# Kernel optimization log

Hardware: AMD Instinct MI355X
Metric: run time of the kernel (lower is better)

The kernel has to match this reference:

```python
import jax, jax.numpy as jnp
import numpy as np

H, DM, DX = 4, 64, 64  # num_heads, out_m_dim, out_x_dim
IN_L, IN_M, IN_X = 128, 128, 128
N, E, E2 = 10000, 160000, 320000


def _edge_softmax(scores, dst, num_nodes):
    # scores: [n_edges, H, 1]; softmax over edges sharing the same dst node
    mx = jax.ops.segment_max(scores, dst, num_segments=num_nodes)
    ex = jnp.exp(scores - mx[dst])
    denom = jax.ops.segment_sum(ex, dst, num_segments=num_nodes)
    return ex / denom[dst]


def setup_inputs() -> dict:
    key = jax.random.key(0)
    ks = jax.random.split(key, 24)

    def xn(k, shape):
        fan = sum(shape)
        return jax.random.normal(k, shape, dtype=jnp.float32) * np.sqrt(2.0 / fan)

    inp = {
        'l_feats': jax.random.normal(ks[0], (N, IN_L), dtype=jnp.float32),
        'm_feats': jax.random.normal(ks[1], (E, IN_M), dtype=jnp.float32),
        'x_feats': jax.random.normal(ks[2], (E2, IN_X), dtype=jnp.float32),
        'g_src': jax.random.randint(ks[3], (E,), 0, N, dtype=jnp.int32),
        'g_dst': jax.random.randint(ks[4], (E,), 0, N, dtype=jnp.int32),
        'lg_src': jax.random.randint(ks[5], (E2,), 0, E, dtype=jnp.int32),
        'lg_dst': jax.random.randint(ks[6], (E2,), 0, E, dtype=jnp.int32),
        # line-graph branch params (torch Linear convention: W [out, in])
        'W_lg_node': xn(ks[7], (DM * H, IN_M + IN_X)),
        'b_lg_node': jnp.zeros((DM * H,), dtype=jnp.float32),
        'W_lg_ni': xn(ks[8], (DX * H, IN_M)),
        'W_lg_fij': xn(ks[9], (DX * H, IN_X)),
        'W_lg_nj': xn(ks[10], (DX * H, IN_M)),
        'lg_attn': xn(ks[11], (1, H, DX)),
        'bias_lg': jnp.zeros((H * DX,), dtype=jnp.float32),
        # base-graph branch params
        'W_g_node': xn(ks[12], (DM * H, IN_M + IN_L)),
        'b_g_node': jnp.zeros((DM * H,), dtype=jnp.float32),
        'W_g_ni': xn(ks[13], (DM * H, IN_L)),
        'W_g_fij': xn(ks[14], (DM * H, IN_M)),
        'W_g_nj': xn(ks[15], (DM * H, IN_L)),
        'g_attn': xn(ks[16], (1, H, DM)),
        'bias_g': jnp.zeros((H * DM,), dtype=jnp.float32),
    }
    return inp


def reference(l_feats, m_feats, x_feats,
              W_lg_node, b_lg_node, W_lg_ni, W_lg_fij, W_lg_nj, lg_attn, bias_lg,
              W_g_node, b_g_node, W_g_ni, W_g_fij, W_g_nj, g_attn, bias_g,
              g_src, g_dst, lg_src, lg_dst):
    n_nodes = l_feats.shape[0]      # graph nodes
    n_lnodes = m_feats.shape[0]     # l_graph nodes == graph edges
    lrelu = jax.nn.leaky_relu       # slope 0.01 (torch default)

    # ---- line-graph attention branch ----
    lg_f_ni = m_feats @ W_lg_ni.T                      # [E, H*DX]
    lg_f_nj = m_feats @ W_lg_nj.T
    lg_f_fij = x_feats @ W_lg_fij.T                    # [E2, H*DX]
    lg_f_out = lrelu(lg_f_ni[lg_src] + lg_f_nj[lg_dst] + lg_f_fij + bias_lg)
    xr = lg_f_out.reshape(-1, H, DX)                   # [E2, H, DX]
    lg_e = jnp.sum(xr * lg_attn, axis=-1, keepdims=True)  # [E2, H, 1]
    a_lg = _edge_softmax(lg_e, lg_dst, n_lnodes)       # [E2, H, 1]

    # mean-aggregate l_graph edge feats onto dst nodes (DGL send_and_recv mean)
    cnt = jax.ops.segment_sum(jnp.ones((lg_dst.shape[0],), dtype=x_feats.dtype),
                              lg_dst, num_segments=n_lnodes)
    agg = jax.ops.segment_sum(x_feats, lg_dst, num_segments=n_lnodes)
    agg = agg / jnp.maximum(cnt, 1.0)[:, None]         # [E, IN_X]

    m1 = jnp.concatenate([m_feats, agg], axis=1)       # [E, IN_M+IN_X]
    h1 = (m1 @ W_lg_node.T + b_lg_node).reshape(-1, H, DM)
    msg1 = h1[lg_src] * a_lg                           # u_mul_e
    h1_dst = jax.ops.segment_sum(msg1, lg_dst, num_segments=n_lnodes)
    lg_h_out = jnp.sum(lrelu(h1_dst), axis=1)          # [E, DM]

    # ---- base-graph attention branch ----
    g_f_ni = l_feats @ W_g_ni.T                        # [N, H*DM]
    g_f_nj = l_feats @ W_g_nj.T
    g_f_fij = m_feats @ W_g_fij.T                      # [E, H*DM]
    g_f_out = lrelu(g_f_ni[g_src] + g_f_nj[g_dst] + g_f_fij + bias_g)
    g_f_out = g_f_out.reshape(-1, H, DM)               # [E, H, DM]
    g_e = jnp.sum(g_f_out * g_attn, axis=-1, keepdims=True)  # [E, H, 1]

    node_edge = l_feats[g_src] + l_feats[g_dst]        # [E, IN_L]
    m2 = jnp.concatenate([node_edge, m_feats], axis=1)  # [E, IN_L+IN_M]
    h2 = (m2 @ W_g_node.T + b_g_node).reshape(-1, H, DM)
    a_g = _edge_softmax(g_e, g_dst, n_nodes)           # [E, H, 1] (per graph edge)
    # l_graph.update_all(u_mul_v): msg[e2] = h2[src(e2)] * a_g[dst(e2)]
    msg2 = h2[lg_src] * a_g[lg_dst]
    h2_dst = jax.ops.segment_sum(msg2, lg_dst, num_segments=n_lnodes)
    g_h_out = jnp.sum(lrelu(h2_dst), axis=1)           # [E, DM]

    return g_h_out + lg_h_out                          # [E, DM]
```

## Files before the change

kernel.cpp:

```cpp
#include <hip/hip_runtime.h>
#include <math.h>

#define LRELU(x) ((x) > 0.0f ? (x) : 0.01f * (x))

typedef __attribute__((ext_vector_type(8))) short short8;
typedef __attribute__((ext_vector_type(4))) float f32x4;

__device__ __forceinline__ unsigned fenc(float f) {
    unsigned u = __float_as_uint(f);
    return (u & 0x80000000u) ? ~u : (u | 0x80000000u);
}
__device__ __forceinline__ float fdec(unsigned u) {
    return __uint_as_float((u & 0x80000000u) ? (u & 0x7FFFFFFFu) : ~u);
}
__device__ __forceinline__ unsigned short f2bf(float f) {
    unsigned u = __float_as_uint(f);
    u += 0x7FFFu + ((u >> 16) & 1u);
    return (unsigned short)(u >> 16);
}
__device__ __forceinline__ float bf2f(unsigned short b) {
    return __uint_as_float(((unsigned)b) << 16);
}
__device__ __forceinline__ ushort4 cvt4(float4 v) {
    ushort4 p;
    p.x = f2bf(v.x); p.y = f2bf(v.y); p.z = f2bf(v.z); p.w = f2bf(v.w);
    return p;
}

__global__ __launch_bounds__(256) void wcvt_k(
    const float* __restrict__ s0, const float* __restrict__ s1,
    const float* __restrict__ s2, const float* __restrict__ s3,
    const float* __restrict__ s4, const float* __restrict__ s5,
    const float* __restrict__ s6, const float* __restrict__ s7,
    unsigned short* __restrict__ dst)
{
    long long e = ((long long)blockIdx.x * 256 + threadIdx.x) * 4;
    if (e >= 327680) return;
    int c = (int)(e >> 15);
    const float* s;
    long long off = e & 32767;
    switch (c) {
        case 0: s = s0; break;
        case 1: s = s1; break;
        case 2: s = s2; break;
        case 3: s = s3; break;
        case 4: s = s4; break;
        case 5: s = s5; break;
        case 6: s = s6; break;
        case 7: s = s6; off += 32768; break;
        case 8: s = s7; break;
        default: s = s7; off += 32768; break;
    }
    float4 v = *(const float4*)&s[off];
    *(ushort4*)&dst[e] = cvt4(v);
}

__global__ __launch_bounds__(256) void cvt1_k(
    const float* __restrict__ in, unsigned short* __restrict__ out, int n4)
{
    int stride = gridDim.x * 256;
    for (int u = blockIdx.x * 256 + threadIdx.x; u < n4; u += stride) {
        float4 v = *(const float4*)&in[(size_t)u * 4];
        *(ushort4*)&out[(size_t)u * 4] = cvt4(v);
    }
}

__device__ __forceinline__ void stage_A128(
    unsigned short* __restrict__ smem, const void* __restrict__ Av, int is_bf16,
    int row0, int M, int tid, int col_off, int stride)
{
    if (is_bf16) {
        const unsigned short* A = (const unsigned short*)Av;
        short8 v[4];
#pragma unroll
        for (int k = 0; k < 4; ++k) {
            int j = tid + k * 256;
            int r = row0 + (j >> 4);
#pragma unroll
            for (int q = 0; q < 8; ++q) v[k][q] = 0;
            if (r < M) v[k] = *(const short8*)&A[(size_t)r * 128 + (j & 15) * 8];
        }
#pragma unroll
        for (int k = 0; k < 4; ++k) {
            int j = tid + k * 256;
            *(short8*)&smem[(j >> 4) * stride + col_off + (j & 15) * 8] = v[k];
        }
    } else {
        const float* A = (const float*)Av;
        float4 va[8];
#pragma unroll
        for (int k = 0; k < 8; ++k) {
            int i = tid + k * 256;
            int r = row0 + (i >> 5);
            va[k] = make_float4(0.f, 0.f, 0.f, 0.f);
            if (r < M) va[k] = *(const float4*)&A[(size_t)r * 128 + (i & 31) * 4];
        }
#pragma unroll
        for (int k = 0; k < 8; ++k) {
            int i = tid + k * 256;
            *(ushort4*)&smem[(i >> 5) * stride + col_off + (i & 31) * 4] = cvt4(va[k]);
        }
    }
}

__global__ __launch_bounds__(256) void gemm128_mfma(
    const void* __restrict__ Av, int a_is_bf16,
    const unsigned short* __restrict__ Wbf,
    const float* __restrict__ biasf, unsigned short* __restrict__ Cout, int M)
{
    __shared__ __align__(16) unsigned short smem[64 * 264];
    const int row0 = blockIdx.x * 64;
    const int tid = threadIdx.x;
    const int wv = tid >> 6, lane = tid & 63;
    const int ln = lane & 15, quad = lane >> 4;

    stage_A128(smem, Av, a_is_bf16, row0, M, tid, 0, 136);
    __syncthreads();

    f32x4 acc[16];
#pragma unroll
    for (int t = 0; t < 16; ++t) acc[t] = (f32x4){0.f, 0.f, 0.f, 0.f};

#pragma unroll 1
    for (int ks = 0; ks < 4; ++ks) {
        short8 a = *(const short8*)&smem[(wv * 16 + ln) * 136 + ks * 32 + quad * 8];
#pragma unroll
        for (int t = 0; t < 16; ++t) {
            short8 b = *(const short8*)&Wbf[(size_t)(t * 16 + ln) * 128 + ks * 32 + quad * 8];
            acc[t] = __builtin_amdgcn_mfma_f32_16x16x32_bf16(a, b, acc[t], 0, 0, 0);
        }
    }
    __syncthreads();

#pragma unroll
    for (int t = 0; t < 16; ++t) {
        int col = t * 16 + ln;
        float bb = biasf ? biasf[col] : 0.0f;
#pragma unroll
        for (int rg = 0; rg < 4; ++rg)
            smem[(wv * 16 + quad * 4 + rg) * 264 + col] = f2bf(acc[t][rg] + bb);
    }
    __syncthreads();
#pragma unroll 1
    for (int i = tid; i < 2048; i += 256) {
        int row = i >> 5, c8 = (i & 31) * 8;
        int r = row0 + row;
        if (r < M) *(short8*)&Cout[(size_t)r * 256 + c8] = *(const short8*)&smem[row * 264 + c8];
    }
}

__global__ __launch_bounds__(256) void gemm_score_mfma(
    const void* __restrict__ Av, int a_is_bf16,
    const unsigned short* __restrict__ Wbf,
    const unsigned short* __restrict__ fni, const unsigned short* __restrict__ fnj,
    const float* __restrict__ bias, const float* __restrict__ attn,
    const int* __restrict__ src, const int* __restrict__ dst,
    float* __restrict__ ebuf, unsigned* __restrict__ smax, int M)
{
    __shared__ __align__(16) unsigned short smem[64 * 264];
    const int row0 = blockIdx.x * 64;
    const int tid = threadIdx.x;
    const int wv = tid >> 6, lane = tid & 63;
    const int ln = lane & 15, quad = lane >> 4;

    const int myr = row0 + wv * 16 + ln;
    int msrc = 0, mdst = 0;
    if (myr < M) { msrc = src[myr]; mdst = dst[myr]; }

    stage_A128(smem, Av, a_is_bf16, row0, M, tid, 0, 136);
    __syncthreads();

    f32x4 acc[16];
#pragma unroll
    for (int t = 0; t < 16; ++t) acc[t] = (f32x4){0.f, 0.f, 0.f, 0.f};

#pragma unroll 1
    for (int ks = 0; ks < 4; ++ks) {
        short8 a = *(const short8*)&smem[(wv * 16 + ln) * 136 + ks * 32 + quad * 8];
#pragma unroll
        for (int t = 0; t < 16; ++t) {
            short8 b = *(const short8*)&Wbf[(size_t)(t * 16 + ln) * 128 + ks * 32 + quad * 8];
            acc[t] = __builtin_amdgcn_mfma_f32_16x16x32_bf16(a, b, acc[t], 0, 0, 0);
        }
    }
    __syncthreads();

    const int c4 = lane * 4;
    const float4 bias4 = *(const float4*)&bias[c4];
    const float4 attn4 = *(const float4*)&attn[c4];

    ushort4 pu[16], pv[16];
#pragma unroll
    for (int j = 0; j < 16; ++j) {
        int s_ = __shfl(msrc, j, 16);
        int d_ = __shfl(mdst, j, 16);
        pu[j] = *(const ushort4*)&fni[(size_t)s_ * 256 + c4];
        pv[j] = *(const ushort4*)&fnj[(size_t)d_ * 256 + c4];
    }

#pragma unroll
    for (int t = 0; t < 16; ++t) {
        int col = t * 16 + ln;
#pragma unroll
        for (int rg = 0; rg < 4; ++rg)
            smem[(wv * 16 + quad * 4 + rg) * 264 + col] = f2bf(acc[t][rg]);
    }
    asm volatile("" ::: "memory");

#pragma unroll
    for (int i = 0; i < 16; ++i) {
        int rr = wv * 16 + i;
        int r = row0 + rr;
        if (r >= M) continue;
        int dIdx = __shfl(mdst, i, 16);
        ushort4 f4 = *(const ushort4*)&smem[rr * 264 + c4];
        float v0 = bf2f(f4.x) + bf2f(pu[i].x) + bf2f(pv[i].x) + bias4.x;
        float v1 = bf2f(f4.y) + bf2f(pu[i].y) + bf2f(pv[i].y) + bias4.y;
        float v2 = bf2f(f4.z) + bf2f(pu[i].z) + bf2f(pv[i].z) + bias4.z;
        float v3 = bf2f(f4.w) + bf2f(pu[i].w) + bf2f(pv[i].w) + bias4.w;
        float p = LRELU(v0) * attn4.x + LRELU(v1) * attn4.y
                + LRELU(v2) * attn4.z + LRELU(v3) * attn4.w;
        p += __shfl_xor(p, 1, 64);
        p += __shfl_xor(p, 2, 64);
        p += __shfl_xor(p, 4, 64);
        p += __shfl_xor(p, 8, 64);
        if (ln == 0) {
            ebuf[(size_t)r * 4 + quad] = p;
            atomicMax(&smax[(size_t)dIdx * 4 + quad], fenc(p));
        }
    }
}

__global__ __launch_bounds__(256) void gemm256_mfma(
    const void* __restrict__ Mv, int m_is_bf16,
    const unsigned short* __restrict__ Aux, const float* __restrict__ lf,
    const int* __restrict__ gsrc, const int* __restrict__ gdst,
    const unsigned short* __restrict__ Wbf, const float* __restrict__ biasf,
    unsigned short* __restrict__ Cout, int M, int mode)
{
    __shared__ __align__(16) unsigned short smem[64 * 264];
    const int row0 = blockIdx.x * 64;
    const int tid = threadIdx.x;
    const int wv = tid >> 6, lane = tid & 63;
    const int ln = lane & 15, quad = lane >> 4;

    if (mode == 0) {
        stage_A128(smem, Mv, m_is_bf16, row0, M, tid, 0, 264);
        stage_A128(smem, Aux, 1, row0, M, tid, 128, 264);
    } else {
        int is[8], id[8];
#pragma unroll
        for (int k = 0; k < 8; ++k) {
            int i = tid + k * 256;
            int r = row0 + (i >> 5);
            is[k] = (r < M) ? gsrc[r] : 0;
            id[k] = (r < M) ? gdst[r] : 0;
        }
        float4 va[8], vb2[8];
#pragma unroll
        for (int k = 0; k < 8; ++k) {
            int i = tid + k * 256;
            int c4i = (i & 31) * 4;
            va[k]  = *(const float4*)&lf[(size_t)is[k] * 128 + c4i];
            vb2[k] = *(const float4*)&lf[(size_t)id[k] * 128 + c4i];
        }
#pragma unroll
        for (int k = 0; k < 8; ++k) {
            int i = tid + k * 256;
            int r = row0 + (i >> 5);
            int c4i = (i & 31) * 4;
            float4 v = make_float4(va[k].x + vb2[k].x, va[k].y + vb2[k].y,
                                   va[k].z + vb2[k].z, va[k].w + vb2[k].w);
            if (r >= M) v = make_float4(0.f, 0.f, 0.f, 0.f);
            *(ushort4*)&smem[(i >> 5) * 264 + c4i] = cvt4(v);
        }
        stage_A128(smem, Mv, m_is_bf16, row0, M, tid, 128, 264);
    }
    __syncthreads();

    f32x4 acc[16];
#pragma unroll
    for (int t = 0; t < 16; ++t) acc[t] = (f32x4){0.f, 0.f, 0.f, 0.f};

#pragma unroll 1
    for (int ks = 0; ks < 8; ++ks) {
        short8 a = *(const short8*)&smem[(wv * 16 + ln) * 264 + ks * 32 + quad * 8];
#pragma unroll
        for (int t = 0; t < 16; ++t) {
            short8 b = *(const short8*)&Wbf[(size_t)(t * 16 + ln) * 256 + ks * 32 + quad * 8];
            acc[t] = __builtin_amdgcn_mfma_f32_16x16x32_bf16(a, b, acc[t], 0, 0, 0);
        }
    }
    __syncthreads();

#pragma unroll
    for (int t = 0; t < 16; ++t) {
        int col = t * 16 + ln;
        float bb = biasf[col];
#pragma unroll
        for (int rg = 0; rg < 4; ++rg)
            smem[(wv * 16 + quad * 4 + rg) * 264 + col] = f2bf(acc[t][rg] + bb);
    }
    __syncthreads();
#pragma unroll 1
    for (int i = tid; i < 2048; i += 256) {
        int row = i >> 5, c8 = (i & 31) * 8;
        int r = row0 + row;
        if (r < M) *(short8*)&Cout[(size_t)r * 256 + c8] = *(const short8*)&smem[row * 264 + c8];
    }
}

__global__ __launch_bounds__(256) void edge_exp(
    float* __restrict__ ebuf, const unsigned* __restrict__ smax,
    float* __restrict__ sden, const int* __restrict__ dst, int nE)
{
    int i = blockIdx.x * 256 + threadIdx.x;
    if (i >= nE * 4) return;
    int e = i >> 2, h = i & 3;
    int d = dst[e];
    float m = fdec(smax[(size_t)d * 4 + h]);
    float ex = expf(ebuf[i] - m);
    ebuf[i] = ex;
    atomicAdd(&sden[(size_t)d * 4 + h], ex);
}

__global__ __launch_bounds__(256) void count_k(
    const int* __restrict__ dst, int* __restrict__ cnt, int n)
{
    int i = blockIdx.x * 256 + threadIdx.x;
    if (i < n) atomicAdd(&cnt[dst[i]], 1);
}

__global__ __launch_bounds__(256) void scan1(
    const int* __restrict__ cnt, int* __restrict__ excl, int* __restrict__ bsum, int n)
{
    __shared__ int sd[256];
    int tid = threadIdx.x;
    int i = blockIdx.x * 256 + tid;
    int v = (i < n) ? cnt[i] : 0;
    sd[tid] = v;
    __syncthreads();
    for (int off2 = 1; off2 < 256; off2 <<= 1) {
        int t = (tid >= off2) ? sd[tid - off2] : 0;
        __syncthreads();
        sd[tid] += t;
        __syncthreads();
    }
    if (i < n) excl[i] = sd[tid] - v;
    if (tid == 255) bsum[blockIdx.x] = sd[255];
}

__global__ __launch_bounds__(1024) void scan2(int* __restrict__ bsum, int nb)
{
    __shared__ int sd[1024];
    int tid = threadIdx.x;
    int v = (tid < nb) ? bsum[tid] : 0;
    sd[tid] = v;
    __syncthreads();
    for (int off2 = 1; off2 < 1024; off2 <<= 1) {
        int t = (tid >= off2) ? sd[tid - off2] : 0;
        __syncthreads();
        sd[tid] += t;
        __syncthreads();
    }
    if (tid < nb) bsum[tid] = sd[tid] - v;
}

__global__ __launch_bounds__(256) void scan3(
    int* __restrict__ excl, const int* __restrict__ bsum, int n, int total)
{
    int i = blockIdx.x * 256 + threadIdx.x;
    if (i < n) excl[i] += bsum[i >> 8];
    if (i == 0) excl[n] = total;
}

__global__ __launch_bounds__(256) void fill_k(
    const int* __restrict__ dst, const int* __restrict__ row_ptr,
    int* __restrict__ cursor, int* __restrict__ colidx, int n)
{
    int i = blockIdx.x * 256 + threadIdx.x;
    if (i >= n) return;
    int d = dst[i];
    int p = atomicAdd(&cursor[d], 1);
    colidx[row_ptr[d] + p] = i;
}

__global__ __launch_bounds__(256) void agg_gather(
    const int* __restrict__ row_ptr, const int* __restrict__ colidx,
    const float* __restrict__ x, unsigned short* __restrict__ aggbf, int nE)
{
    const int lane = threadIdx.x & 63;
    const int d = blockIdx.x * 4 + (threadIdx.x >> 6);
    if (d >= nE) return;
    int b = row_ptr[d], en = row_ptr[d + 1];
    float s0 = 0.f, s1 = 0.f;
    for (int k0 = b; k0 < en; k0 += 4) {
        const int cnt = (en - k0 < 4) ? (en - k0) : 4;
        int e[4];
#pragma unroll
        for (int j = 0; j < 4; ++j)
            e[j] = (j < cnt) ? colidx[k0 + j] : 0;
        float2 v[4];
#pragma unroll
        for (int j = 0; j < 4; ++j) {
            v[j] = make_float2(0.f, 0.f);
            if (j < cnt)
                v[j] = *(const float2*)&x[(size_t)e[j] * 128 + lane * 2];
        }
#pragma unroll
        for (int j = 0; j < 4; ++j) { s0 += v[j].x; s1 += v[j].y; }
    }
    float c = fmaxf((float)(en - b), 1.0f);
    ushort2 o;
    o.x = f2bf(s0 / c); o.y = f2bf(s1 / c);
    *(ushort2*)&aggbf[(size_t)d * 128 + lane * 2] = o;
}

__global__ __launch_bounds__(256) void final_agg(
    const int* __restrict__ row_ptr, const int* __restrict__ colidx,
    const int* __restrict__ lg_src, const float* __restrict__ e_lg,
    const unsigned* __restrict__ lgmax,
    const unsigned short* __restrict__ h1, const unsigned short* __restrict__ h2,
    const float* __restrict__ e_g, const float* __restrict__ gden,
    const int* __restrict__ g_dst, float* __restrict__ out, int nE)
{
    const int lane = threadIdx.x & 63;
    const int d = blockIdx.x * 4 + (threadIdx.x >> 6);
    if (d >= nE) return;
    int b = row_ptr[d], en = row_ptr[d + 1];

    uint4 mu = *(const uint4*)&lgmax[(size_t)d * 4];
    float mx0 = fdec(mu.x), mx1 = fdec(mu.y), mx2 = fdec(mu.z), mx3 = fdec(mu.w);

    float den0 = 0.f, den1 = 0.f, den2 = 0.f, den3 = 0.f;
    float a10 = 0.f, a11 = 0.f, a12 = 0.f, a13 = 0.f;
    float a20 = 0.f, a21 = 0.f, a22 = 0.f, a23 = 0.f;

    for (int k0 = b; k0 < en; k0 += 4) {
        const int cnt = (en - k0 < 4) ? (en - k0) : 4;
        int e[4];
#pragma unroll
        for (int j = 0; j < 4; ++j)
            e[j] = (j < cnt) ? colidx[k0 + j] : 0;

        float4 sc[4];
        int s[4];
#pragma unroll
        for (int j = 0; j < 4; ++j) {
            sc[j] = make_float4(0.f, 0.f, 0.f, 0.f);
            s[j] = 0;
            if (j < cnt) {
                sc[j] = *(const float4*)&e_lg[(size_t)e[j] * 4];
                s[j] = lg_src[e[j]];
            }
        }

        ushort4 r1v[4], r2v[4];
#pragma unroll
        for (int j = 0; j < 4; ++j) {
            r1v[j] = make_ushort4(0, 0, 0, 0);
            r2v[j] = make_ushort4(0, 0, 0, 0);
            if (j < cnt) {
                const unsigned short* p1 = &h1[(size_t)s[j] * 256 + lane];
                const unsigned short* p2 = &h2[(size_t)s[j] * 256 + lane];
                r1v[j].x = p1[0];   r1v[j].y = p1[64];
                r1v[j].z = p1[128]; r1v[j].w = p1[192];
                r2v[j].x = p2[0];   r2v[j].y = p2[64];
                r2v[j].z = p2[128]; r2v[j].w = p2[192];
            }
        }

#pragma unroll
        for (int j = 0; j < 4; ++j) {
            if (j < cnt) {
                float w0 = expf(sc[j].x - mx0), w1 = expf(sc[j].y - mx1);
                float w2 = expf(sc[j].z - mx2), w3 = expf(sc[j].w - mx3);
                den0 += w0; den1 += w1; den2 += w2; den3 += w3;
                a10 += bf2f(r1v[j].x) * w0;
                a11 += bf2f(r1v[j].y) * w1;
                a12 += bf2f(r1v[j].z) * w2;
                a13 += bf2f(r1v[j].w) * w3;
                a20 += bf2f(r2v[j].x);
                a21 += bf2f(r2v[j].y);
                a22 += bf2f(r2v[j].z);
                a23 += bf2f(r2v[j].w);
            }
        }
    }

    float o = 0.f;
    if (en > b) {
        float v0 = a10 / den0, v1 = a11 / den1, v2 = a12 / den2, v3 = a13 / den3;
        o += LRELU(v0) + LRELU(v1) + LRELU(v2) + LRELU(v3);
    }
    int gd = g_dst[d];
    float g0 = e_g[(size_t)d * 4 + 0] / gden[(size_t)gd * 4 + 0] * a20;
    float g1 = e_g[(size_t)d * 4 + 1] / gden[(size_t)gd * 4 + 1] * a21;
    float g2 = e_g[(size_t)d * 4 + 2] / gden[(size_t)gd * 4 + 2] * a22;
    float g3 = e_g[(size_t)d * 4 + 3] / gden[(size_t)gd * 4 + 3] * a23;
    o += LRELU(g0) + LRELU(g1) + LRELU(g2) + LRELU(g3);
    out[(size_t)d * 64 + lane] = o;
}

extern "C" void kernel_launch(void* const* d_in, const int* in_sizes, int n_in,
                              void* d_out, int out_size, void* d_ws, size_t ws_size,
                              hipStream_t stream)
{
    const float* l_feats   = (const float*)d_in[0];
    const float* m_feats   = (const float*)d_in[1];
    const float* x_feats   = (const float*)d_in[2];
    const int*   g_src     = (const int*)d_in[3];
    const int*   g_dst     = (const int*)d_in[4];
    const int*   lg_src    = (const int*)d_in[5];
    const int*   lg_dst    = (const int*)d_in[6];
    const float* W_lg_node = (const float*)d_in[7];
    const float* b_lg_node = (const float*)d_in[8];
    const float* W_lg_ni   = (const float*)d_in[9];
    const float* W_lg_fij  = (const float*)d_in[10];
    const float* W_lg_nj   = (const float*)d_in[11];
    const float* lg_attn   = (const float*)d_in[12];
    const float* bias_lg   = (const float*)d_in[13];
    const float* W_g_node  = (const float*)d_in[14];
    const float* b_g_node  = (const float*)d_in[15];
    const float* W_g_ni    = (const float*)d_in[16];
    const float* W_g_fij   = (const float*)d_in[17];
    const float* W_g_nj    = (const float*)d_in[18];
    const float* g_attn    = (const float*)d_in[19];
    const float* bias_g    = (const float*)d_in[20];

    const int N  = in_sizes[0] / 128;
    const int E  = in_sizes[3];
    const int E2 = in_sizes[5];

    float* ws = (float*)d_ws;
    size_t off = 0;
    auto alloc = [&](size_t n) { float* p = ws + off; off += n; return p; };

    unsigned short* wbuf = (unsigned short*)alloc(163840);
    unsigned short* wgni_bf    = wbuf;
    unsigned short* wgnj_bf    = wbuf + 32768;
    unsigned short* wlgni_bf   = wbuf + 65536;
    unsigned short* wlgnj_bf   = wbuf + 98304;
    unsigned short* wlgfij_bf  = wbuf + 131072;
    unsigned short* wgfij_bf   = wbuf + 163840;
    unsigned short* wlgnode_bf = wbuf + 196608;
    unsigned short* wgnode_bf  = wbuf + 262144;

    unsigned short* ni_lg = (unsigned short*)alloc((size_t)E * 128);
    unsigned short* nj_lg = (unsigned short*)alloc((size_t)E * 128);
    unsigned short* gni   = (unsigned short*)alloc((size_t)N * 128);
    unsigned short* gnj   = (unsigned short*)alloc((size_t)N * 128);
    unsigned short* aggbf = (unsigned short*)alloc((size_t)E * 64);
    float* e_lg  = alloc((size_t)E2 * 4);
    float* e_g   = alloc((size_t)E * 4);
    unsigned* gmax = (unsigned*)alloc((size_t)N * 4);
    float* gden  = alloc((size_t)N * 4);
    unsigned* lgmax = (unsigned*)alloc((size_t)E * 4);
    int* row_ptr = (int*)alloc((size_t)E + 4);
    int* colidx  = (int*)alloc((size_t)E2);
    int* cnt     = (int*)alloc((size_t)E);
    int* cursor  = (int*)alloc((size_t)E);
    int* bsum    = (int*)alloc(1024);

    const int use_mbf = ((off + (size_t)E * 64) * sizeof(float) <= ws_size) ? 1 : 0;
    unsigned short* mbf = use_mbf ? (unsigned short*)alloc((size_t)E * 64) : nullptr;
    const void* mA = use_mbf ? (const void*)mbf : (const void*)m_feats;

    unsigned short* h1 = ni_lg;
    unsigned short* h2 = nj_lg;

    (void)n_in; (void)out_size;
    float* outp = (float*)d_out;
    dim3 blk(256);

    hipMemsetAsync(cnt,    0, (size_t)E * 4, stream);
    hipMemsetAsync(cursor, 0, (size_t)E * 4, stream);
    hipMemsetAsync(gmax,   0, (size_t)N * 4 * 4, stream);
    hipMemsetAsync(gden,   0, (size_t)N * 4 * 4, stream);
    hipMemsetAsync(lgmax,  0, (size_t)E * 4 * 4, stream);

    wcvt_k<<<320, blk, 0, stream>>>(W_g_ni, W_g_nj, W_lg_ni, W_lg_nj,
                                    W_lg_fij, W_g_fij, W_lg_node, W_g_node, wbuf);
    if (use_mbf)
        cvt1_k<<<2048, blk, 0, stream>>>(m_feats, mbf, E * 32);

    const int nb = (E + 255) / 256;
    count_k<<<(E2 + 255) / 256, blk, 0, stream>>>(lg_dst, cnt, E2);
    scan1<<<nb, blk, 0, stream>>>(cnt, row_ptr, bsum, E);
    scan2<<<1, 1024, 0, stream>>>(bsum, nb);
    scan3<<<nb, blk, 0, stream>>>(row_ptr, bsum, E, E2);
    fill_k<<<(E2 + 255) / 256, blk, 0, stream>>>(lg_dst, row_ptr, cursor, colidx, E2);

    gemm128_mfma<<<(N + 63) / 64, blk, 0, stream>>>(l_feats, 0, wgni_bf, nullptr, gni, N);
    gemm128_mfma<<<(N + 63) / 64, blk, 0, stream>>>(l_feats, 0, wgnj_bf, nullptr, gnj, N);
    gemm128_mfma<<<(E + 63) / 64, blk, 0, stream>>>(mA, use_mbf, wlgni_bf, nullptr, ni_lg, E);
    gemm128_mfma<<<(E + 63) / 64, blk, 0, stream>>>(mA, use_mbf, wlgnj_bf, nullptr, nj_lg, E);

    gemm_score_mfma<<<(E2 + 63) / 64, blk, 0, stream>>>(
        x_feats, 0, wlgfij_bf, ni_lg, nj_lg, bias_lg, lg_attn, lg_src, lg_dst,
        e_lg, lgmax, E2);
    gemm_score_mfma<<<(E + 63) / 64, blk, 0, stream>>>(
        mA, use_mbf, wgfij_bf, gni, gnj, bias_g, g_attn, g_src, g_dst,
        e_g, gmax, E);

    edge_exp<<<(unsigned)(((long long)E * 4 + 255) / 256), blk, 0, stream>>>(e_g, gmax, gden, g_dst, E);

    agg_gather<<<(E + 3) / 4, blk, 0, stream>>>(row_ptr, colidx, x_feats, aggbf, E);

    gemm256_mfma<<<(E + 63) / 64, blk, 0, stream>>>(
        mA, use_mbf, aggbf, nullptr, nullptr, nullptr, wlgnode_bf, b_lg_node, h1, E, 0);
    gemm256_mfma<<<(E + 63) / 64, blk, 0, stream>>>(
        mA, use_mbf, nullptr, l_feats, g_src, g_dst, wgnode_bf, b_g_node, h2, E, 1);

    final_agg<<<(E + 3) / 4, blk, 0, stream>>>(
        row_ptr, colidx, lg_src, e_lg, lgmax, h1, h2, e_g, gden, g_dst, outp, E);
}
```

Measured before the change: 1.416 ms.

## Merge projection, score and node GEMM launches into combined dual-section kernels

The four 128-wide projection GEMMs become one kernel in which each block stages its A tile once and computes both ni and nj outputs from a paired weight buffer. Its epilogue uses per-wave shared staging with no block barriers. The two score GEMMs and the two 256-wide node GEMMs are each merged into a single launch, with the block index choosing the section. The aim is to halve A-tile reads for the projections, cut launch count and tail effects, and let small grids overlap large ones. The cost is more branching on block index and heavier per-block work in the projection kernel.

Result: no change. 1.427 ms (+0.8%).

```diff
diff --git a/kernel.cpp b/kernel.cpp
--- a/kernel.cpp
+++ b/kernel.cpp
@@ -103,65 +103,102 @@
     }
 }
 
-__global__ __launch_bounds__(256) void gemm128_mfma(
-    const void* __restrict__ Av, int a_is_bf16,
-    const unsigned short* __restrict__ Wbf,
-    const float* __restrict__ biasf, unsigned short* __restrict__ Cout, int M)
-{
-    __shared__ __align__(16) unsigned short smem[64 * 264];
-    const int row0 = blockIdx.x * 64;
+__global__ __launch_bounds__(256) void proj_dual(
+    const void* __restrict__ A0v, int bf0, const unsigned short* __restrict__ W0,
+    unsigned short* __restrict__ C0a, unsigned short* __restrict__ C0b, int M0, int nblk0,
+    const void* __restrict__ A1v, int bf1, const unsigned short* __restrict__ W1,
+    unsigned short* __restrict__ C1a, unsigned short* __restrict__ C1b, int M1)
+{
+    __shared__ __align__(16) unsigned short stg[64 * 136];
+    __shared__ __align__(16) unsigned short sth[4][16 * 132];
     const int tid = threadIdx.x;
     const int wv = tid >> 6, lane = tid & 63;
     const int ln = lane & 15, quad = lane >> 4;
 
-    stage_A128(smem, Av, a_is_bf16, row0, M, tid, 0, 136);
-    __syncthreads();
-
-    f32x4 acc[16];
-#pragma unroll
-    for (int t = 0; t < 16; ++t) acc[t] = (f32x4){0.f, 0.f, 0.f, 0.f};
+    const int sec = (blockIdx.x >= (unsigned)nblk0) ? 1 : 0;
+    const void* Av = sec ? A1v : A0v;
+    const int a_is_bf16 = sec ? bf1 : bf0;
+    const unsigned short* Wbf = sec ? W1 : W0;
+    const int M = sec ? M1 : M0;
+    const int row0 = (sec ? (blockIdx.x - nblk0) : blockIdx.x) * 64;
+
+    stage_A128(stg, Av, a_is_bf16, row0, M, tid, 0, 136);
+    __syncthreads();
 
 #pragma unroll 1
-    for (int ks = 0; ks < 4; ++ks) {
-        short8 a = *(const short8*)&smem[(wv * 16 + ln) * 136 + ks * 32 + quad * 8];
-#pragma unroll
-        for (int t = 0; t < 16; ++t) {
-            short8 b = *(const short8*)&Wbf[(size_t)(t * 16 + ln) * 128 + ks * 32 + quad * 8];
-            acc[t] = __builtin_amdgcn_mfma_f32_16x16x32_bf16(a, b, acc[t], 0, 0, 0);
-        }
-    }
-    __syncthreads();
-
-#pragma unroll
-    for (int t = 0; t < 16; ++t) {
-        int col = t * 16 + ln;
-        float bb = biasf ? biasf[col] : 0.0f;
-#pragma unroll
-        for (int rg = 0; rg < 4; ++rg)
-            smem[(wv * 16 + quad * 4 + rg) * 264 + col] = f2bf(acc[t][rg] + bb);
-    }
-    __syncthreads();
+    for (int h = 0; h < 2; ++h) {
+        f32x4 acc[16];
+#pragma unroll
+        for (int t = 0; t < 16; ++t) acc[t] = (f32x4){0.f, 0.f, 0.f, 0.f};
+        const unsigned short* W = Wbf + (size_t)h * 256 * 128;
+
 #pragma unroll 1
-    for (int i = tid; i < 2048; i += 256) {
-        int row = i >> 5, c8 = (i & 31) * 8;
-        int r = row0 + row;
-        if (r < M) *(short8*)&Cout[(size_t)r * 256 + c8] = *(const short8*)&smem[row * 264 + c8];
-    }
-}
-
-__global__ __launch_bounds__(256) void gemm_score_mfma(
-    const void* __restrict__ Av, int a_is_bf16,
-    const unsigned short* __restrict__ Wbf,
-    const unsigned short* __restrict__ fni, const unsigned short* __restrict__ fnj,
-    const float* __restrict__ bias, const float* __restrict__ attn,
-    const int* __restrict__ src, const int* __restrict__ dst,
-    float* __restrict__ ebuf, unsigned* __restrict__ smax, int M)
+        for (int ks = 0; ks < 4; ++ks) {
+            short8 a = *(const short8*)&stg[(wv * 16 + ln) * 136 + ks * 32 + quad * 8];
+#pragma unroll
+            for (int t = 0; t < 16; ++t) {
+                short8 b = *(const short8*)&W[(size_t)(t * 16 + ln) * 128 + ks * 32 + quad * 8];
+                acc[t] = __builtin_amdgcn_mfma_f32_16x16x32_bf16(a, b, acc[t], 0, 0, 0);
+            }
+        }
+
+        unsigned short* C = h ? (sec ? C1b : C0b) : (sec ? C1a : C0a);
+#pragma unroll 1
+        for (int ch = 0; ch < 2; ++ch) {
+#pragma unroll
+            for (int tt = 0; tt < 8; ++tt) {
+                int t = ch * 8 + tt;
+                int col = tt * 16 + ln;
+#pragma unroll
+                for (int rg = 0; rg < 4; ++rg)
+                    sth[wv][(quad * 4 + rg) * 132 + col] = f2bf(acc[t][rg]);
+            }
+            asm volatile("" ::: "memory");
+#pragma unroll
+            for (int k = 0; k < 4; ++k) {
+                int j = lane + k * 64;
+                int row = j >> 4, c8 = (j & 15) * 8;
+                int r = row0 + wv * 16 + row;
+                if (r < M)
+                    *(short8*)&C[(size_t)r * 256 + ch * 128 + c8] =
+                        *(const short8*)&sth[wv][row * 132 + c8];
+            }
+            asm volatile("" ::: "memory");
+        }
+    }
+}
+
+__global__ __launch_bounds__(256) void gemm_score2(
+    const void* __restrict__ A0v, int bf0, const unsigned short* __restrict__ W0,
+    const unsigned short* __restrict__ fni0, const unsigned short* __restrict__ fnj0,
+    const float* __restrict__ bias0, const float* __restrict__ attn0,
+    const int* __restrict__ src0, const int* __restrict__ dst0,
+    float* __restrict__ ebuf0, unsigned* __restrict__ smax0, int M0, int nblk0,
+    const void* __restrict__ A1v, int bf1, const unsigned short* __restrict__ W1,
+    const unsigned short* __restrict__ fni1, const unsigned short* __restrict__ fnj1,
+    const float* __restrict__ bias1, const float* __restrict__ attn1,
+    const int* __restrict__ src1, const int* __restrict__ dst1,
+    float* __restrict__ ebuf1, unsigned* __restrict__ smax1, int M1)
 {
     __shared__ __align__(16) unsigned short smem[64 * 264];
-    const int row0 = blockIdx.x * 64;
     const int tid = threadIdx.x;
     const int wv = tid >> 6, lane = tid & 63;
     const int ln = lane & 15, quad = lane >> 4;
+
+    const int sec = (blockIdx.x >= (unsigned)nblk0) ? 1 : 0;
+    const void* Av = sec ? A1v : A0v;
+    const int a_is_bf16 = sec ? bf1 : bf0;
+    const unsigned short* Wbf = sec ? W1 : W0;
+    const unsigned short* fni = sec ? fni1 : fni0;
+    const unsigned short* fnj = sec ? fnj1 : fnj0;
+    const float* bias = sec ? bias1 : bias0;
+    const float* attn = sec ? attn1 : attn0;
+    const int* src = sec ? src1 : src0;
+    const int* dst = sec ? dst1 : dst0;
+    float* ebuf = sec ? ebuf1 : ebuf0;
+    unsigned* smax = sec ? smax1 : smax0;
+    const int M = sec ? M1 : M0;
+    const int row0 = (sec ? (blockIdx.x - nblk0) : blockIdx.x) * 64;
 
     const int myr = row0 + wv * 16 + ln;
     int msrc = 0, mdst = 0;
@@ -235,14 +272,21 @@
     const void* __restrict__ Mv, int m_is_bf16,
     const unsigned short* __restrict__ Aux, const float* __restrict__ lf,
     const int* __restrict__ gsrc, const int* __restrict__ gdst,
-    const unsigned short* __restrict__ Wbf, const float* __restrict__ biasf,
-    unsigned short* __restrict__ Cout, int M, int mode)
+    const unsigned short* __restrict__ W0, const float* __restrict__ b0,
+    unsigned short* __restrict__ C0,
+    const unsigned short* __restrict__ W1, const float* __restrict__ b1,
+    unsigned short* __restrict__ C1, int M, int nblk0)
 {
     __shared__ __align__(16) unsigned short smem[64 * 264];
-    const int row0 = blockIdx.x * 64;
     const int tid = threadIdx.x;
     const int wv = tid >> 6, lane = tid & 63;
     const int ln = lane & 15, quad = lane >> 4;
+
+    const int mode = (blockIdx.x >= (unsigned)nblk0) ? 1 : 0;
+    const unsigned short* Wbf = mode ? W1 : W0;
+    const float* biasf = mode ? b1 : b0;
+    unsigned short* Cout = mode ? C1 : C0;
+    const int row0 = (mode ? (blockIdx.x - nblk0) : blockIdx.x) * 64;
 
     if (mode == 0) {
         stage_A128(smem, Mv, m_is_bf16, row0, M, tid, 0, 264);
@@ -537,10 +581,8 @@
     auto alloc = [&](size_t n) { float* p = ws + off; off += n; return p; };
 
     unsigned short* wbuf = (unsigned short*)alloc(163840);
-    unsigned short* wgni_bf    = wbuf;
-    unsigned short* wgnj_bf    = wbuf + 32768;
-    unsigned short* wlgni_bf   = wbuf + 65536;
-    unsigned short* wlgnj_bf   = wbuf + 98304;
+    unsigned short* wgni_pair  = wbuf;
+    unsigned short* wlgni_pair = wbuf + 65536;
     unsigned short* wlgfij_bf  = wbuf + 131072;
     unsigned short* wgfij_bf   = wbuf + 163840;
     unsigned short* wlgnode_bf = wbuf + 196608;
@@ -591,15 +633,17 @@
     scan3<<<nb, blk, 0, stream>>>(row_ptr, bsum, E, E2);
     fill_k<<<(E2 + 255) / 256, blk, 0, stream>>>(lg_dst, row_ptr, cursor, colidx, E2);
 
-    gemm128_mfma<<<(N + 63) / 64, blk, 0, stream>>>(l_feats, 0, wgni_bf, nullptr, gni, N);
-    gemm128_mfma<<<(N + 63) / 64, blk, 0, stream>>>(l_feats, 0, wgnj_bf, nullptr, gnj, N);
-    gemm128_mfma<<<(E + 63) / 64, blk, 0, stream>>>(mA, use_mbf, wlgni_bf, nullptr, ni_lg, E);
-    gemm128_mfma<<<(E + 63) / 64, blk, 0, stream>>>(mA, use_mbf, wlgnj_bf, nullptr, nj_lg, E);
-
-    gemm_score_mfma<<<(E2 + 63) / 64, blk, 0, stream>>>(
+    const int pb0 = (E + 63) / 64;
+    const int pb1 = (N + 63) / 64;
+    proj_dual<<<pb0 + pb1, blk, 0, stream>>>(
+        mA, use_mbf, wlgni_pair, ni_lg, nj_lg, E, pb0,
+        l_feats, 0, wgni_pair, gni, gnj, N);
+
+    const int sb0 = (E2 + 63) / 64;
+    const int sb1 = (E + 63) / 64;
+    gemm_score2<<<sb0 + sb1, blk, 0, stream>>>(
         x_feats, 0, wlgfij_bf, ni_lg, nj_lg, bias_lg, lg_attn, lg_src, lg_dst,
-        e_lg, lgmax, E2);
-    gemm_score_mfma<<<(E + 63) / 64, blk, 0, stream>>>(
+        e_lg, lgmax, E2, sb0,
         mA, use_mbf, wgfij_bf, gni, gnj, bias_g, g_attn, g_src, g_dst,
         e_g, gmax, E);
 
@@ -607,10 +651,11 @@
 
     agg_gather<<<(E + 3) / 4, blk, 0, stream>>>(row_ptr, colidx, x_feats, aggbf, E);
 
-    gemm256_mfma<<<(E + 63) / 64, blk, 0, stream>>>(
-        mA, use_mbf, aggbf, nullptr, nullptr, nullptr, wlgnode_bf, b_lg_node, h1, E, 0);
-    gemm256_mfma<<<(E + 63) / 64, blk, 0, stream>>>(
-        mA, use_mbf, nullptr, l_feats, g_src, g_dst, wgnode_bf, b_g_node, h2, E, 1);
+    const int gb = (E + 63) / 64;
+    gemm256_mfma<<<gb * 2, blk, 0, stream>>>(
+        mA, use_mbf, aggbf, l_feats, g_src, g_dst,
+        wlgnode_bf, b_lg_node, h1,
+        wgnode_bf, b_g_node, h2, E, gb);
 
     final_agg<<<(E + 3) / 4, blk, 0, stream>>>(
         row_ptr, colidx, lg_src, e_lg, lgmax, h1, h2, e_g, gden, g_dst, outp, E);
```
